# Performance work log

Measured on AMD Instinct MI355X. Metric: run time of the kernel, lower is better.

The kernel has to match this reference:

```python
import jax, jax.numpy as jnp
import numpy as np

D_MODEL = 1024
N_HEADS = 16
HEAD_DIM = D_MODEL // N_HEADS  # 64, rope_dim == head_dim
D_FF = 4096
BATCH = 2
SEQ = 2048
EPS = 1e-6


def setup_inputs() -> dict:
    key = jax.random.key(0)
    ks = jax.random.split(key, 12)
    x = jax.random.normal(ks[0], (BATCH, SEQ, D_MODEL), dtype=jnp.float32)
    # realistic RoPE angles: theta = pos * inv_freq, duplicated to fill rope_dim
    half = HEAD_DIM // 2
    inv_freq = 1.0 / (10000.0 ** (jnp.arange(0, half, dtype=jnp.float32) / half))
    pos = jnp.arange(SEQ, dtype=jnp.float32)
    freqs = pos[:, None] * inv_freq[None, :]              # [S, half]
    rotary_pos_emb = jnp.concatenate([freqs, freqs], axis=-1)[:, None, :]  # [S,1,64]
    s = D_MODEL ** -0.5
    wq = jax.random.normal(ks[1], (D_MODEL, D_MODEL), dtype=jnp.float32) * s
    wk = jax.random.normal(ks[2], (D_MODEL, D_MODEL), dtype=jnp.float32) * s
    wv = jax.random.normal(ks[3], (D_MODEL, D_MODEL), dtype=jnp.float32) * s
    wo = jax.random.normal(ks[4], (D_MODEL, D_MODEL), dtype=jnp.float32) * s
    w_gate = jax.random.normal(ks[5], (D_FF, D_MODEL), dtype=jnp.float32) * s
    w_up = jax.random.normal(ks[6], (D_FF, D_MODEL), dtype=jnp.float32) * s
    w_down = jax.random.normal(ks[7], (D_MODEL, D_FF), dtype=jnp.float32) * (D_FF ** -0.5)
    norm1_w = jnp.ones((D_MODEL,), dtype=jnp.float32)
    norm2_w = jnp.ones((D_MODEL,), dtype=jnp.float32)
    return {"x": x, "rotary_pos_emb": rotary_pos_emb, "wq": wq, "wk": wk,
            "wv": wv, "wo": wo, "w_gate": w_gate, "w_up": w_up,
            "w_down": w_down, "norm1_w": norm1_w, "norm2_w": norm2_w}


def _rms_norm(x, w):
    # torch: x / (||x||/sqrt(d) + eps) * w  (eps added to the norm, not variance)
    norm = jnp.linalg.norm(x, axis=-1, keepdims=True) * (x.shape[-1] ** -0.5)
    return x / (norm + EPS) * w


def _rotate_half(t):
    t1, t2 = jnp.split(t, 2, axis=-1)
    return jnp.concatenate([-t2, t1], axis=-1)


def _apply_rope(t, cos, sin):
    # t: [B,H,S,D]; cos/sin: [S,D] broadcast over batch/heads
    return t * cos[None, None] + _rotate_half(t) * sin[None, None]


def reference(x, rotary_pos_emb, wq, wk, wv, wo, w_gate, w_up, w_down, norm1_w, norm2_w):
    B, S, _ = x.shape
    H, D = N_HEADS, HEAD_DIM

    # ---- attention sublayer ----
    residual = x
    h = _rms_norm(x, norm1_w)
    q = (h @ wq.T).reshape(B, S, H, D).transpose(0, 2, 1, 3)  # [B,H,S,D]
    k = (h @ wk.T).reshape(B, S, H, D).transpose(0, 2, 1, 3)
    v = (h @ wv.T).reshape(B, S, H, D).transpose(0, 2, 1, 3)

    freqs = rotary_pos_emb[:, 0, :]  # [S, D] (rope_dim == head_dim)
    cos, sin = jnp.cos(freqs), jnp.sin(freqs)
    q = _apply_rope(q, cos, sin)
    k = _apply_rope(k, cos, sin)

    scores = jnp.einsum('bhsd,bhtd->bhst', q, k) / jnp.sqrt(jnp.float32(D))
    causal = jnp.tril(jnp.ones((S, S), dtype=bool))  # True = keep
    scores = jnp.where(causal[None, None], scores, jnp.finfo(scores.dtype).min)
    attn = jax.nn.softmax(scores, axis=-1)  # dropout is identity in eval
    attn_out = jnp.einsum('bhst,bhtd->bhsd', attn, v)
    attn_out = attn_out.transpose(0, 2, 1, 3).reshape(B, S, H * D)
    x = residual + attn_out @ wo.T

    # ---- SwiGLU MLP sublayer ----
    residual = x
    h = _rms_norm(x, norm2_w)
    gate = h @ w_gate.T
    up = h @ w_up.T
    ff = (jax.nn.silu(gate) * up) @ w_down.T
    return residual + ff
```

## Files before the change

### kernel.cpp

```cpp
#include <hip/hip_runtime.h>

typedef __bf16 bf16;
typedef __attribute__((ext_vector_type(8))) __bf16 bf16x8;
typedef __attribute__((ext_vector_type(4))) float f32x4;

#define B_SZ 2
#define SEQ 2048
#define DM 1024
#define NH 16
#define HD 64
#define DFF 4096
#define NROWS (B_SZ*SEQ)

__device__ __forceinline__ f32x4 mfma16(bf16x8 a, bf16x8 b, f32x4 c) {
    return __builtin_amdgcn_mfma_f32_16x16x32_bf16(a, b, c, 0, 0, 0);
}

__device__ __forceinline__ void gload16(const bf16* g, bf16* l) {
    __builtin_amdgcn_global_load_lds(
        (const __attribute__((address_space(1))) void*)g,
        (__attribute__((address_space(3))) void*)l, 16, 0, 0);
}


__global__ __launch_bounds__(256) void convert_all_k(
    const float* __restrict__ wq, const float* __restrict__ wk,
    const float* __restrict__ wv, const float* __restrict__ wo,
    const float* __restrict__ wg, const float* __restrict__ wu,
    const float* __restrict__ wd,
    bf16* __restrict__ wqkvb, bf16* __restrict__ wob,
    bf16* __restrict__ wgub, bf16* __restrict__ wdb) {
    const long M1 = 1l << 20;
    long i = ((long)blockIdx.x * 256 + threadIdx.x) * 8;
    const float* src; bf16* dst; long off;
    if (i < 3 * M1) {
        int sct = (int)(i >> 20);
        src = sct == 0 ? wq : (sct == 1 ? wk : wv);
        off = i & (M1 - 1); dst = wqkvb + i;
    } else if (i < 4 * M1) {
        src = wo; off = i - 3 * M1; dst = wob + off;
    } else if (i < 12 * M1) {
        long j = i - 4 * M1;
        int fr = (int)(j >> 10), c = (int)(j & 1023);
        int g = fr >> 6, r = fr & 63;
        int f = g * 32 + (r & 31);
        src = (r & 32) ? wu : wg; off = (long)f * 1024 + c; dst = wgub + j;
    } else {
        src = wd; off = i - 12 * M1; dst = wdb + off;
    }
    float4 v0 = *(const float4*)(src + off);
    float4 v1 = *(const float4*)(src + off + 4);
    dst[0] = (bf16)v0.x; dst[1] = (bf16)v0.y; dst[2] = (bf16)v0.z; dst[3] = (bf16)v0.w;
    dst[4] = (bf16)v1.x; dst[5] = (bf16)v1.y; dst[6] = (bf16)v1.z; dst[7] = (bf16)v1.w;
}

__global__ __launch_bounds__(256) void rope_table_k(const float* __restrict__ rope,
                                                    float* __restrict__ ct,
                                                    float* __restrict__ st) {
    int i = blockIdx.x * 256 + threadIdx.x;
    int sI = i >> 5, d = i & 31;
    float f = rope[sI * 64 + d];
    ct[i] = cosf(f);
    st[i] = sinf(f);
}

__global__ __launch_bounds__(256) void rmsnorm_k(const float* __restrict__ x,
                                                 const float* __restrict__ w,
                                                 bf16* __restrict__ o) {
    int row = blockIdx.x;
    int tid = threadIdx.x;
    float4 v = ((const float4*)(x + (long)row * DM))[tid];
    float ss = v.x*v.x + v.y*v.y + v.z*v.z + v.w*v.w;
    #pragma unroll
    for (int off = 32; off >= 1; off >>= 1) ss += __shfl_xor(ss, off, 64);
    __shared__ float sred[4];
    if ((tid & 63) == 0) sred[tid >> 6] = ss;
    __syncthreads();
    float tot = sred[0] + sred[1] + sred[2] + sred[3];
    float scale = 1.f / (sqrtf(tot * (1.f / (float)DM)) + 1e-6f);
    float4 wv = ((const float4*)w)[tid];
    bf16* orow = o + (long)row * DM + tid * 4;
    orow[0] = (bf16)(v.x * scale * wv.x);
    orow[1] = (bf16)(v.y * scale * wv.y);
    orow[2] = (bf16)(v.z * scale * wv.z);
    orow[3] = (bf16)(v.w * scale * wv.w);
}


template<int EPI>
__global__ __launch_bounds__(512, 2)
void gemm256(const bf16* __restrict__ A, const bf16* __restrict__ W,
             int K, bf16* __restrict__ o1, bf16* __restrict__ o2,
             bf16* __restrict__ o3,
             const float* __restrict__ ct, const float* __restrict__ st) {
    __shared__ __align__(16) char smem[131072];
    bf16* Ah = (bf16*)smem;
    bf16* Bh = (bf16*)(smem + 65536);
    const int tid = threadIdx.x;
    const int wid = tid >> 6, l = tid & 63;
    const int lr = l & 15, lg = l >> 4;
    const int wr = wid >> 2, wcn = wid & 3;
    const int nwg = gridDim.x * gridDim.y;
    const int orig = blockIdx.y * gridDim.x + blockIdx.x;
    const int swz = (orig & 7) * (nwg >> 3) + (orig >> 3);
    const int bx = swz % gridDim.x, by = swz / gridDim.x;
    const long mbase = (long)bx * 256;
    const long nbase = (long)by * 256;

    f32x4 acc[8][4] = {};
    const int nk = K >> 6;
    const int P = nk * 2;

    const int aoff0 = lr * 64 + ((wr * 4 + lg) ^ (lr & 7)) * 8;
    const int boff0 = ((wcn & 1) * 64 + lr) * 64 + (((wcn >> 1) * 4 + lg) ^ (lr & 7)) * 8;

    auto stageHalf = [&](int ph) {
        const int buf = ph & 3, h = ph & 1, kt = ph >> 1;
        bf16* abase = Ah + buf * 8192;
        bf16* bbase = Bh + buf * 8192;
        const long kcol = (long)kt * 64 + h * 32;
        #pragma unroll
        for (int i = 0; i < 2; ++i) {
            int s = i * 512 + tid;
            int prow = s >> 3, pblk = s & 7;
            int L = pblk ^ (prow & 7);
            long gr = (long)((L >> 2) * 128 + prow);
            long gc = kcol + (L & 3) * 8;
            gload16(&A[(mbase + gr) * K + gc], abase + s * 8);
            gload16(&W[(nbase + gr) * K + gc], bbase + s * 8);
        }
    };

    auto computeHalf = [&](int ph) {
        const int buf = ph & 3;
        const bf16* abase = Ah + buf * 8192;
        const bf16* bbase = Bh + buf * 8192;
        bf16x8 bfr[4];
        #pragma unroll
        for (int ni = 0; ni < 4; ++ni)
            bfr[ni] = *(const bf16x8*)&bbase[ni * 1024 + boff0];
        #pragma unroll
        for (int ms = 0; ms < 2; ++ms) {
            bf16x8 af[4];
            #pragma unroll
            for (int mi = 0; mi < 4; ++mi)
                af[mi] = *(const bf16x8*)&abase[(ms * 4 + mi) * 1024 + aoff0];
            __builtin_amdgcn_s_setprio(1);
            #pragma unroll
            for (int mi = 0; mi < 4; ++mi)
                #pragma unroll
                for (int ni = 0; ni < 4; ++ni)
                    acc[ms * 4 + mi][ni] = mfma16(af[mi], bfr[ni], acc[ms * 4 + mi][ni]);
            __builtin_amdgcn_s_setprio(0);
        }
    };

    stageHalf(0);
    stageHalf(1);
    stageHalf(2);
    for (int p = 0; p < P; ++p) {
        if (p < P - 2)       asm volatile("s_waitcnt vmcnt(8)" ::: "memory");
        else if (p == P - 2) asm volatile("s_waitcnt vmcnt(4)" ::: "memory");
        else                 asm volatile("s_waitcnt vmcnt(0)" ::: "memory");
        __builtin_amdgcn_s_barrier();
        __builtin_amdgcn_sched_barrier(0);
        if (p + 3 < P) stageHalf(p + 3);
        computeHalf(p);
    }

    if (EPI == 0) {
        const long colW = nbase + wcn * 64;
        const int sect = (int)(colW >> 10);
        const int hh = (int)((colW >> 6) & 15);
        #pragma unroll
        for (int a = 0; a < 8; ++a) {
            #pragma unroll
            for (int nn = 0; nn < 2; ++nn) {
                const int dd = nn * 16 + lr;
                #pragma unroll
                for (int r = 0; r < 4; ++r) {
                    long row = mbase + wr * 128 + a * 16 + 4 * lg + r;
                    int b = (int)(row >> 11), s = (int)(row & 2047);
                    float v1 = acc[a][nn][r];
                    float v2 = acc[a][nn + 2][r];
                    if (sect < 2) {
                        if (sect == 0) { v1 *= 0.125f; v2 *= 0.125f; }
                        float c = ct[s * 32 + dd], sn = st[s * 32 + dd];
                        bf16* dst = (sect == 0) ? o1 : o2;
                        long pth = (((long)(b * NH + hh) * SEQ + s) << 6) + dd;
                        dst[pth]      = (bf16)(v1 * c - v2 * sn);
                        dst[pth + 32] = (bf16)(v2 * c + v1 * sn);
                    } else {
                        long pth = ((long)(b * NH + hh) * HD + dd) * SEQ + s;
                        o3[pth]            = (bf16)v1;
                        o3[pth + 32 * SEQ] = (bf16)v2;
                    }
                }
            }
        }
    }

    if (EPI == 3) {
        const int fb = (int)(nbase + wcn * 64) >> 1;
        #pragma unroll
        for (int a = 0; a < 8; ++a)
            #pragma unroll
            for (int ni = 0; ni < 2; ++ni)
                #pragma unroll
                for (int r = 0; r < 4; ++r) {
                    long row = mbase + wr * 128 + a * 16 + 4 * lg + r;
                    float g = acc[a][ni][r];
                    float u = acc[a][ni + 2][r];
                    float sg = g / (1.f + __expf(-g));
                    o1[row * 4096 + fb + ni * 16 + lr] = (bf16)(sg * u);
                }
    }
}


__global__ __launch_bounds__(512, 4)
void gemm64x128(const bf16* __restrict__ A, const bf16* __restrict__ W,
                int K, int N, const float* __restrict__ resid, float* __restrict__ of) {
    __shared__ bf16 As[3][64 * 64];
    __shared__ bf16 Bs[3][128 * 64];
    const int tid = threadIdx.x;
    const int wid = tid >> 6, l = tid & 63;
    const int lr = l & 15, lg = l >> 4;
    const int wr = wid >> 2, wcn = wid & 3;
    const long mbase = (long)blockIdx.x * 64;
    const long nbase = (long)blockIdx.y * 128;

    f32x4 acc[2][2] = {};
    const int nk = K >> 6;

    auto stage = [&](int b, int kt) {
        {
            int s = tid;
            int row = s >> 3, pblk = s & 7;
            int L = pblk ^ (row & 7);
            gload16(&A[(mbase + row) * K + kt * 64 + L * 8], &As[b][s * 8]);
        }
        #pragma unroll
        for (int i = 0; i < 2; ++i) {
            int s = i * 512 + tid;
            int row = s >> 3, pblk = s & 7;
            int L = pblk ^ (row & 7);
            gload16(&W[(nbase + row) * K + kt * 64 + L * 8], &Bs[b][s * 8]);
        }
    };
    auto compute = [&](int b) {
        #pragma unroll
        for (int kk = 0; kk < 2; ++kk) {
            bf16x8 af[2], bfr[2];
            #pragma unroll
            for (int mi = 0; mi < 2; ++mi) {
                int row = wr * 32 + mi * 16 + lr;
                af[mi] = *(const bf16x8*)&As[b][row * 64 + ((kk * 4 + lg) ^ (lr & 7)) * 8];
            }
            #pragma unroll
            for (int ni = 0; ni < 2; ++ni) {
                int row = wcn * 32 + ni * 16 + lr;
                bfr[ni] = *(const bf16x8*)&Bs[b][row * 64 + ((kk * 4 + lg) ^ (lr & 7)) * 8];
            }
            __builtin_amdgcn_s_setprio(1);
            #pragma unroll
            for (int mi = 0; mi < 2; ++mi)
                #pragma unroll
                for (int ni = 0; ni < 2; ++ni)
                    acc[mi][ni] = mfma16(af[mi], bfr[ni], acc[mi][ni]);
            __builtin_amdgcn_s_setprio(0);
        }
    };

    stage(0, 0);
    stage(1, 1);
    for (int kt = 0; kt < nk; ++kt) {
        if (kt < nk - 1) asm volatile("s_waitcnt vmcnt(3)" ::: "memory");
        else             asm volatile("s_waitcnt vmcnt(0)" ::: "memory");
        __builtin_amdgcn_s_barrier();
        __builtin_amdgcn_sched_barrier(0);
        if (kt + 2 < nk) stage((kt + 2) % 3, kt + 2);
        compute(kt % 3);
    }

    #pragma unroll
    for (int mi = 0; mi < 2; ++mi)
        #pragma unroll
        for (int ni = 0; ni < 2; ++ni)
            #pragma unroll
            for (int r = 0; r < 4; ++r) {
                long row = mbase + wr * 32 + mi * 16 + 4 * lg + r;
                long col = nbase + wcn * 32 + ni * 16 + lr;
                of[row * N + col] = resid[row * N + col] + acc[mi][ni][r];
            }
}


__device__ __forceinline__ void attn_tile(
    int tb, int qw, bool diag,
    const bf16x8& qf0, const bf16x8& qf1,
    const bf16* Kl, const bf16* Vl, bf16* Plw,
    int lr, int lg, f32x4* oacc, float* mr, f32x4& lacc)
{
    f32x4 s[4];
    __builtin_amdgcn_s_setprio(1);
    #pragma unroll
    for (int tf = 0; tf < 4; ++tf) {
        f32x4 z = {0.f, 0.f, 0.f, 0.f};
        bf16x8 k0 = *(const bf16x8*)&Kl[(tf * 16 + lr) * 64 + ((0 + lg) ^ (lr & 7)) * 8];
        bf16x8 k1 = *(const bf16x8*)&Kl[(tf * 16 + lr) * 64 + ((4 + lg) ^ (lr & 7)) * 8];
        z = mfma16(qf0, k0, z);
        z = mfma16(qf1, k1, z);
        s[tf] = z;
    }
    __builtin_amdgcn_s_setprio(0);

    float pv[4][4];
    float pmax[4] = {-1e30f, -1e30f, -1e30f, -1e30f};
    #pragma unroll
    for (int tf = 0; tf < 4; ++tf) {
        int t = tb + tf * 16 + lr;
        #pragma unroll
        for (int r = 0; r < 4; ++r) {
            float sv = s[tf][r];
            if (diag && t > qw + 4 * lg + r) sv = -1e30f;
            pv[tf][r] = sv;
            pmax[r] = fmaxf(pmax[r], sv);
        }
    }
    #pragma unroll
    for (int r = 0; r < 4; ++r) {
        pmax[r] = fmaxf(pmax[r], __shfl_xor(pmax[r], 8, 64));
        pmax[r] = fmaxf(pmax[r], __shfl_xor(pmax[r], 4, 64));
        pmax[r] = fmaxf(pmax[r], __shfl_xor(pmax[r], 2, 64));
        pmax[r] = fmaxf(pmax[r], __shfl_xor(pmax[r], 1, 64));
    }
    bool within = (pmax[0] <= mr[0] + 8.f) && (pmax[1] <= mr[1] + 8.f) &&
                  (pmax[2] <= mr[2] + 8.f) && (pmax[3] <= mr[3] + 8.f);
    if (!__all(within)) {
        float alpha[4];
        #pragma unroll
        for (int r = 0; r < 4; ++r) {
            float mn = fmaxf(mr[r], pmax[r]);
            alpha[r] = __expf(mr[r] - mn);
            mr[r] = mn;
        }
        #pragma unroll
        for (int r = 0; r < 4; ++r) lacc[r] *= alpha[r];
        #pragma unroll
        for (int df = 0; df < 4; ++df) {
            f32x4 t4 = oacc[df];
            t4[0] *= alpha[0]; t4[1] *= alpha[1];
            t4[2] *= alpha[2]; t4[3] *= alpha[3];
            oacc[df] = t4;
        }
    }
    #pragma unroll
    for (int tf = 0; tf < 4; ++tf)
        #pragma unroll
        for (int r = 0; r < 4; ++r)
            Plw[(4 * lg + r) * 68 + tf * 16 + lr] = (bf16)__expf(pv[tf][r] - mr[r]);

    bf16x8 pa0, pa1;
    #pragma unroll
    for (int j = 0; j < 8; ++j) {
        pa0[j] = Plw[lr * 68 + lg * 8 + j];
        pa1[j] = Plw[lr * 68 + 32 + lg * 8 + j];
    }
    bf16x8 ones;
    #pragma unroll
    for (int j = 0; j < 8; ++j) ones[j] = (bf16)1.0f;
    __builtin_amdgcn_s_setprio(1);
    lacc = mfma16(pa0, ones, lacc);
    lacc = mfma16(pa1, ones, lacc);
    #pragma unroll
    for (int df = 0; df < 4; ++df) {
        bf16x8 v0 = *(const bf16x8*)&Vl[(df * 16 + lr) * 64 + ((0 + lg) ^ (lr & 7)) * 8];
        bf16x8 v1 = *(const bf16x8*)&Vl[(df * 16 + lr) * 64 + ((4 + lg) ^ (lr & 7)) * 8];
        oacc[df] = mfma16(pa0, v0, oacc[df]);
        oacc[df] = mfma16(pa1, v1, oacc[df]);
    }
    __builtin_amdgcn_s_setprio(0);
}

__global__ __launch_bounds__(256)
void attn_fwd(const bf16* __restrict__ q, const bf16* __restrict__ k,
              const bf16* __restrict__ vt, bf16* __restrict__ o) {
    __shared__ bf16 Kl[2][64 * 64];
    __shared__ bf16 Vl[2][64 * 64];
    __shared__ bf16 Pl[4][16 * 68];
    const int tid = threadIdx.x, wid = tid >> 6, l = tid & 63;
    const int lr = l & 15, lg = l >> 4;
    const int qtA = blockIdx.x;
    const int qtB = 31 - qtA;
    const int bh = blockIdx.y;
    const long kbase = (long)bh * SEQ * HD;
    const long vbase = (long)bh * HD * SEQ;
    const int qwA = qtA * 64 + wid * 16;
    const int qwB = qtB * 64 + wid * 16;

    bf16x8 qA0, qA1, qB0, qB1;
    {
        const bf16* qp = q + kbase + (long)(qwA + lr) * HD + lg * 8;
        qA0 = *(const bf16x8*)qp; qA1 = *(const bf16x8*)(qp + 32);
        const bf16* qp2 = q + kbase + (long)(qwB + lr) * HD + lg * 8;
        qB0 = *(const bf16x8*)qp2; qB1 = *(const bf16x8*)(qp2 + 32);
    }
    f32x4 oA[4] = {}, oB[4] = {};
    f32x4 lA = {0.f, 0.f, 0.f, 0.f}, lB = {0.f, 0.f, 0.f, 0.f};
    float mA[4] = {-1e30f, -1e30f, -1e30f, -1e30f};
    float mB[4] = {-1e30f, -1e30f, -1e30f, -1e30f};

    auto stageKV = [&](int b, int tb) {
        #pragma unroll
        for (int i = 0; i < 4; ++i) {
            int slot = i * 256 + tid;
            int row = (slot >> 3) & 63;
            int bs = (slot & 7) ^ (row & 7);
            if (slot < 512)
                gload16(&k[kbase + (long)(tb + row) * HD + bs * 8], &Kl[b][slot * 8]);
            else
                gload16(&vt[vbase + (long)row * SEQ + tb + bs * 8], &Vl[b][(slot - 512) * 8]);
        }
    };

    const int nt = qtB + 1;
    stageKV(0, 0);
    __syncthreads();
    int cur = 0;
    for (int tb_i = 0; tb_i < nt; ++tb_i) {
        const int tb = tb_i * 64;
        if (tb_i + 1 < nt) stageKV(cur ^ 1, tb + 64);
        if (tb_i <= qtA)
            attn_tile(tb, qwA, tb_i == qtA, qA0, qA1, Kl[cur], Vl[cur], Pl[wid], lr, lg, oA, mA, lA);
        attn_tile(tb, qwB, tb_i == qtB, qB0, qB1, Kl[cur], Vl[cur], Pl[wid], lr, lg, oB, mB, lB);
        __syncthreads();
        cur ^= 1;
    }

    const int b = bh >> 4, h = bh & 15;
    #pragma unroll
    for (int df = 0; df < 4; ++df) {
        #pragma unroll
        for (int r = 0; r < 4; ++r) {
            int sA = qwA + 4 * lg + r;
            int sB = qwB + 4 * lg + r;
            o[((long)(b * SEQ + sA) * DM) + h * HD + df * 16 + lr] = (bf16)(oA[df][r] / lA[r]);
            o[((long)(b * SEQ + sB) * DM) + h * HD + df * 16 + lr] = (bf16)(oB[df][r] / lB[r]);
        }
    }
}


extern "C" void kernel_launch(void* const* d_in, const int* in_sizes, int n_in,
                              void* d_out, int out_size, void* d_ws, size_t ws_size,
                              hipStream_t stream) {
    (void)in_sizes; (void)n_in; (void)out_size; (void)ws_size;
    const float* x    = (const float*)d_in[0];
    const float* rope = (const float*)d_in[1];
    const float* wq   = (const float*)d_in[2];
    const float* wk   = (const float*)d_in[3];
    const float* wv   = (const float*)d_in[4];
    const float* wo   = (const float*)d_in[5];
    const float* wg   = (const float*)d_in[6];
    const float* wu   = (const float*)d_in[7];
    const float* wd   = (const float*)d_in[8];
    const float* n1w  = (const float*)d_in[9];
    const float* n2w  = (const float*)d_in[10];
    float* out = (float*)d_out;

    char* ws = (char*)d_ws;
    const size_t MB = 1u << 20;
    bf16* wqkvb = (bf16*)(ws + 0 * MB);
    bf16* wob   = (bf16*)(ws + 6 * MB);
    bf16* wgub  = (bf16*)(ws + 8 * MB);
    bf16* wdb   = (bf16*)(ws + 24 * MB);
    bf16* hb    = (bf16*)(ws + 32 * MB);
    bf16* qb_   = (bf16*)(ws + 40 * MB);
    bf16* kb_   = (bf16*)(ws + 56 * MB);
    bf16* vtb   = (bf16*)(ws + 72 * MB);
    bf16* attnb = (bf16*)(ws + 88 * MB);
    float* x2   = (float*)(ws + 40 * MB);
    bf16* midb  = (bf16*)(ws + 56 * MB);
    float* ctab = (float*)(ws + 104 * MB);
    float* stab = (float*)(ws + 104 * MB + (1u << 18));

    convert_all_k<<<8192, 256, 0, stream>>>(wq, wk, wv, wo, wg, wu, wd,
                                            wqkvb, wob, wgub, wdb);
    rope_table_k<<<256, 256, 0, stream>>>(rope, ctab, stab);

    rmsnorm_k<<<NROWS, 256, 0, stream>>>(x, n1w, hb);

    gemm256<0><<<dim3(16, 12), 512, 0, stream>>>(hb, wqkvb, DM, qb_, kb_, vtb, ctab, stab);

    attn_fwd<<<dim3(16, 32), 256, 0, stream>>>(qb_, kb_, vtb, attnb);

    gemm64x128<<<dim3(64, 8), 512, 0, stream>>>(attnb, wob, DM, DM, x, x2);

    rmsnorm_k<<<NROWS, 256, 0, stream>>>(x2, n2w, hb);

    gemm256<3><<<dim3(16, 32), 512, 0, stream>>>(hb, wgub, DM, midb, nullptr, nullptr, nullptr, nullptr);

    gemm64x128<<<dim3(64, 8), 512, 0, stream>>>(midb, wdb, DFF, DM, x2, out);
}
```

Baseline: 296.0 us.

## Fold log2e into Q scale, use exp2 softmax, vectorize P reads and one-wave rmsnorm

Measured after the change: 297.8 us. Within noise of the previous version (+0.6%).

```diff
diff --git a/kernel.cpp b/kernel.cpp
--- a/kernel.cpp
+++ b/kernel.cpp
@@ -11,6 +11,9 @@
 #define HD 64
 #define DFF 4096
 #define NROWS (B_SZ*SEQ)
+
+#define QSCALE 0.18033688f
+#define DEFER_THR 11.541561f
 
 __device__ __forceinline__ f32x4 mfma16(bf16x8 a, bf16x8 b, f32x4 c) {
     return __builtin_amdgcn_mfma_f32_16x16x32_bf16(a, b, c, 0, 0, 0);
@@ -67,23 +70,30 @@
 __global__ __launch_bounds__(256) void rmsnorm_k(const float* __restrict__ x,
                                                  const float* __restrict__ w,
                                                  bf16* __restrict__ o) {
-    int row = blockIdx.x;
-    int tid = threadIdx.x;
-    float4 v = ((const float4*)(x + (long)row * DM))[tid];
-    float ss = v.x*v.x + v.y*v.y + v.z*v.z + v.w*v.w;
+    const int wv = threadIdx.x >> 6, l = threadIdx.x & 63;
+    const long row = (long)blockIdx.x * 4 + wv;
+    const float4* xr = (const float4*)(x + row * DM);
+    float4 v[4];
+    float ss = 0.f;
+    #pragma unroll
+    for (int j = 0; j < 4; ++j) {
+        v[j] = xr[l + j * 64];
+        ss += v[j].x*v[j].x + v[j].y*v[j].y + v[j].z*v[j].z + v[j].w*v[j].w;
+    }
     #pragma unroll
     for (int off = 32; off >= 1; off >>= 1) ss += __shfl_xor(ss, off, 64);
-    __shared__ float sred[4];
-    if ((tid & 63) == 0) sred[tid >> 6] = ss;
-    __syncthreads();
-    float tot = sred[0] + sred[1] + sred[2] + sred[3];
-    float scale = 1.f / (sqrtf(tot * (1.f / (float)DM)) + 1e-6f);
-    float4 wv = ((const float4*)w)[tid];
-    bf16* orow = o + (long)row * DM + tid * 4;
-    orow[0] = (bf16)(v.x * scale * wv.x);
-    orow[1] = (bf16)(v.y * scale * wv.y);
-    orow[2] = (bf16)(v.z * scale * wv.z);
-    orow[3] = (bf16)(v.w * scale * wv.w);
+    float scale = 1.f / (sqrtf(ss * (1.f / (float)DM)) + 1e-6f);
+    bf16* orow = o + row * DM;
+    #pragma unroll
+    for (int j = 0; j < 4; ++j) {
+        float4 wv4 = ((const float4*)w)[l + j * 64];
+        bf16 t[4];
+        t[0] = (bf16)(v[j].x * scale * wv4.x);
+        t[1] = (bf16)(v[j].y * scale * wv4.y);
+        t[2] = (bf16)(v[j].z * scale * wv4.z);
+        t[3] = (bf16)(v[j].w * scale * wv4.w);
+        *(short4*)(orow + (l + j * 64) * 4) = *(short4*)t;
+    }
 }
 
 
@@ -184,7 +194,7 @@
                     float v1 = acc[a][nn][r];
                     float v2 = acc[a][nn + 2][r];
                     if (sect < 2) {
-                        if (sect == 0) { v1 *= 0.125f; v2 *= 0.125f; }
+                        if (sect == 0) { v1 *= QSCALE; v2 *= QSCALE; }
                         float c = ct[s * 32 + dd], sn = st[s * 32 + dd];
                         bf16* dst = (sect == 0) ? o1 : o2;
                         long pth = (((long)(b * NH + hh) * SEQ + s) << 6) + dd;
@@ -335,14 +345,14 @@
         pmax[r] = fmaxf(pmax[r], __shfl_xor(pmax[r], 2, 64));
         pmax[r] = fmaxf(pmax[r], __shfl_xor(pmax[r], 1, 64));
     }
-    bool within = (pmax[0] <= mr[0] + 8.f) && (pmax[1] <= mr[1] + 8.f) &&
-                  (pmax[2] <= mr[2] + 8.f) && (pmax[3] <= mr[3] + 8.f);
+    bool within = (pmax[0] <= mr[0] + DEFER_THR) && (pmax[1] <= mr[1] + DEFER_THR) &&
+                  (pmax[2] <= mr[2] + DEFER_THR) && (pmax[3] <= mr[3] + DEFER_THR);
     if (!__all(within)) {
         float alpha[4];
         #pragma unroll
         for (int r = 0; r < 4; ++r) {
             float mn = fmaxf(mr[r], pmax[r]);
-            alpha[r] = __expf(mr[r] - mn);
+            alpha[r] = exp2f(mr[r] - mn);
             mr[r] = mn;
         }
         #pragma unroll
@@ -359,14 +369,10 @@
     for (int tf = 0; tf < 4; ++tf)
         #pragma unroll
         for (int r = 0; r < 4; ++r)
-            Plw[(4 * lg + r) * 68 + tf * 16 + lr] = (bf16)__expf(pv[tf][r] - mr[r]);
-
-    bf16x8 pa0, pa1;
-    #pragma unroll
-    for (int j = 0; j < 8; ++j) {
-        pa0[j] = Plw[lr * 68 + lg * 8 + j];
-        pa1[j] = Plw[lr * 68 + 32 + lg * 8 + j];
-    }
+            Plw[(4 * lg + r) * 72 + tf * 16 + lr] = (bf16)exp2f(pv[tf][r] - mr[r]);
+
+    bf16x8 pa0 = *(const bf16x8*)&Plw[lr * 72 + lg * 8];
+    bf16x8 pa1 = *(const bf16x8*)&Plw[lr * 72 + 32 + lg * 8];
     bf16x8 ones;
     #pragma unroll
     for (int j = 0; j < 8; ++j) ones[j] = (bf16)1.0f;
@@ -388,7 +394,7 @@
               const bf16* __restrict__ vt, bf16* __restrict__ o) {
     __shared__ bf16 Kl[2][64 * 64];
     __shared__ bf16 Vl[2][64 * 64];
-    __shared__ bf16 Pl[4][16 * 68];
+    __shared__ bf16 Pl[4][16 * 72];
     const int tid = threadIdx.x, wid = tid >> 6, l = tid & 63;
     const int lr = l & 15, lg = l >> 4;
     const int qtA = blockIdx.x;
@@ -489,7 +495,7 @@
                                             wqkvb, wob, wgub, wdb);
     rope_table_k<<<256, 256, 0, stream>>>(rope, ctab, stab);
 
-    rmsnorm_k<<<NROWS, 256, 0, stream>>>(x, n1w, hb);
+    rmsnorm_k<<<NROWS / 4, 256, 0, stream>>>(x, n1w, hb);
 
     gemm256<0><<<dim3(16, 12), 512, 0, stream>>>(hb, wqkvb, DM, qb_, kb_, vtb, ctab, stab);
 
@@ -497,7 +503,7 @@
 
     gemm64x128<<<dim3(64, 8), 512, 0, stream>>>(attnb, wob, DM, DM, x, x2);
 
-    rmsnorm_k<<<NROWS, 256, 0, stream>>>(x2, n2w, hb);
+    rmsnorm_k<<<NROWS / 4, 256, 0, stream>>>(x2, n2w, hb);
 
     gemm256<3><<<dim3(16, 32), 512, 0, stream>>>(hb, wgub, DM, midb, nullptr, nullptr, nullptr, nullptr);
 
```
